# Performance work log

Hardware: AMD Instinct MI355X
Metric: run time of the kernel (lower is better)

The kernel has to match this reference:

```python
import jax, jax.numpy as jnp
import numpy as np
from jax import lax

D = 1024
N_EXP = 8
DD = 4 * D
BS = 8192
TRAIN_CAP = 1.0
LN_EPS = 1e-5


def setup_inputs() -> dict:
    key = jax.random.key(0)
    ks = jax.random.split(key, 8)
    s = 0.02
    return {
        "x": jax.random.normal(ks[0], (BS, D), jnp.float32),
        "Wg": jax.random.normal(ks[1], (N_EXP, D), jnp.float32) * s,
        "cp_w1": jax.random.normal(ks[2], (D, D), jnp.float32) * s,
        "cp_b1": jnp.zeros((D,), jnp.float32),
        "cp_w2": jax.random.normal(ks[3], (N_EXP, D), jnp.float32) * s,
        "cp_b2": jnp.zeros((N_EXP,), jnp.float32),
        "ln_g": jnp.ones((D,), jnp.float32),
        "ln_b": jnp.zeros((D,), jnp.float32),
        "fc1s": jax.random.normal(ks[4], (N_EXP, DD, D), jnp.float32) * s,
        "b1s": jnp.zeros((N_EXP, DD), jnp.float32),
        "fc2s": jax.random.normal(ks[5], (N_EXP, D, DD), jnp.float32) * s,
        "b2s": jnp.zeros((N_EXP, D), jnp.float32),
    }


def reference(x, Wg, cp_w1, cp_b1, cp_w2, cp_b2, ln_g, ln_b, fc1s, b1s, fc2s, b2s):
    bs, d = x.shape
    n = Wg.shape[0]
    k = int(bs * TRAIN_CAP) // n  # tokens kept per expert

    # gate scores in (0,1): (tanh(x Wg^T)+1)/2   -> [bs, n]
    scores = (jnp.tanh(x @ Wg.T) + 1.0) * 0.5

    # per-expert descending sort of tokens by score
    order = jnp.argsort(-scores, axis=0)                      # [bs, n]
    sorted_w = jnp.take_along_axis(scores, order, axis=0)     # [bs, n]
    kept_w = sorted_w[:k]                                     # [k, n]
    kept_idx = order[:k]                                      # [k, n]

    # keep mask (labels for capacity predictor)
    keep_mask = jnp.zeros((bs, n), x.dtype).at[kept_idx, jnp.arange(n)[None, :]].set(1.0)

    # capacity predictor loss (BCE with logits, x detached)
    xd = lax.stop_gradient(x)
    h = jax.nn.gelu(xd @ cp_w1.T + cp_b1, approximate=True)
    logits = h @ cp_w2.T + cp_b2                              # [bs, n]
    cap_loss = jnp.mean(jnp.logaddexp(0.0, logits) - logits * keep_mask)

    # dispatch: gather selected tokens, row-major flatten of [k, n]
    idx = kept_idx.reshape(-1)                                # [k*n]
    y = x[idx]                                                # [k*n, d]

    # LayerNorm
    mu = y.mean(-1, keepdims=True)
    var = y.var(-1, keepdims=True)
    y = (y - mu) * lax.rsqrt(var + LN_EPS) * ln_g + ln_b

    # per-expert grouped GEMMs
    y3 = y.reshape(k, n, d)
    h1 = jnp.einsum('knd,nfd->knf', y3, fc1s) + b1s[None]     # [k, n, dd]
    h1 = jax.nn.gelu(h1, approximate=True)
    y2 = jnp.einsum('knf,ndf->knd', h1, fc2s) + b2s[None]     # [k, n, d]

    # weight by gate score and scatter-add back (residual)
    y2 = y2 * kept_w[..., None]
    out = x.at[idx].add(y2.reshape(k * n, d))
    return out, cap_loss
```

## Files before the change

kernel.cpp:

```cpp
#include <hip/hip_runtime.h>


#define BS_   8192
#define D_    1024
#define DD_   4096
#define NEXP  8
#define KCAP  1024

typedef unsigned int   uint32;
typedef unsigned short u16;
typedef __bf16 bf16x8  __attribute__((ext_vector_type(8)));
typedef float  f32x4   __attribute__((ext_vector_type(4)));
typedef u16    u16x8   __attribute__((ext_vector_type(8)));
typedef u16    u16x4   __attribute__((ext_vector_type(4)));

__device__ __forceinline__ u16 f2bf(float f){
  uint32 u = __float_as_uint(f);
  u = (u + 0x7fffu + ((u >> 16) & 1u)) >> 16;
  return (u16)u;
}
__device__ __forceinline__ float bf_lo(uint32 u){ return __uint_as_float(u << 16); }
__device__ __forceinline__ float bf_hi(uint32 u){ return __uint_as_float(u & 0xffff0000u); }

__device__ __forceinline__ float gelu_fast(float v){
  const float u2 = v * (1.5957691216057308f + 0.07135481282962162f * v * v);
  const float e  = __expf(u2);
  return v - v / (1.0f + e);
}
__device__ __forceinline__ void glds16(const u16* g, u16* l){
  __builtin_amdgcn_global_load_lds(
      (const __attribute__((address_space(1))) unsigned int*)g,
      (__attribute__((address_space(3))) unsigned int*)l, 16, 0, 0);
}

__global__ __launch_bounds__(256)
void pack_b_kernel(const float* __restrict__ in, u16* __restrict__ out,
                   int K, int kshift)
{
  const long long t = (long long)blockIdx.x * 256 + threadIdx.x;
  const int  lane  = (int)(t & 63);
  const long long brick = t >> 6;
  const long long n16 = brick >> kshift;
  const int  k32  = (int)(brick & ((1 << kshift) - 1));
  const float* src = in + (n16 * 16 + (lane & 15)) * (long long)K
                        + k32 * 32 + (lane >> 4) * 8;
  const float4 a = *(const float4*)src;
  const float4 b = *(const float4*)(src + 4);
  u16x8 o;
  o[0]=f2bf(a.x); o[1]=f2bf(a.y); o[2]=f2bf(a.z); o[3]=f2bf(a.w);
  o[4]=f2bf(b.x); o[5]=f2bf(b.y); o[6]=f2bf(b.z); o[7]=f2bf(b.w);
  *(u16x8*)(out + t * 8) = o;
}

__global__ __launch_bounds__(64)
void gating_kernel(const float* __restrict__ x, const float* __restrict__ Wg,
                   float* __restrict__ scores, uint32* __restrict__ keep_bits,
                   u16* __restrict__ xh)
{
  const int i    = blockIdx.x;
  const int lane = threadIdx.x;
  const float* xr = x + (size_t)i * D_ + lane * 16;
  const float4 x0 = *(const float4*)(xr +  0);
  const float4 x1 = *(const float4*)(xr +  4);
  const float4 x2 = *(const float4*)(xr +  8);
  const float4 x3 = *(const float4*)(xr + 12);
  u16x8 p0, p1;
  p0[0]=f2bf(x0.x); p0[1]=f2bf(x0.y); p0[2]=f2bf(x0.z); p0[3]=f2bf(x0.w);
  p0[4]=f2bf(x1.x); p0[5]=f2bf(x1.y); p0[6]=f2bf(x1.z); p0[7]=f2bf(x1.w);
  p1[0]=f2bf(x2.x); p1[1]=f2bf(x2.y); p1[2]=f2bf(x2.z); p1[3]=f2bf(x2.w);
  p1[4]=f2bf(x3.x); p1[5]=f2bf(x3.y); p1[6]=f2bf(x3.z); p1[7]=f2bf(x3.w);
  u16* dst = xh + ((size_t)(i >> 4) * 32 + (lane >> 1)) * 512
                + (lane & 1) * 256 + (i & 15) * 8;
  *(u16x8*)dst         = p0;
  *(u16x8*)(dst + 128) = p1;

  float acc[NEXP];
  #pragma unroll
  for (int e = 0; e < NEXP; e++){
    const float* wr = Wg + e * D_ + lane * 16;
    const float4 w0 = *(const float4*)(wr +  0);
    const float4 w1 = *(const float4*)(wr +  4);
    const float4 w2 = *(const float4*)(wr +  8);
    const float4 w3 = *(const float4*)(wr + 12);
    float s = x0.x*w0.x + x0.y*w0.y + x0.z*w0.z + x0.w*w0.w;
    s += x1.x*w1.x + x1.y*w1.y + x1.z*w1.z + x1.w*w1.w;
    s += x2.x*w2.x + x2.y*w2.y + x2.z*w2.z + x2.w*w2.w;
    s += x3.x*w3.x + x3.y*w3.y + x3.z*w3.z + x3.w*w3.w;
    acc[e] = s;
  }
  #pragma unroll
  for (int e = 0; e < NEXP; e++){
    #pragma unroll
    for (int off = 32; off >= 1; off >>= 1) acc[e] += __shfl_xor(acc[e], off);
  }
  if (lane == 0){
    #pragma unroll
    for (int e = 0; e < NEXP; e++) scores[i * NEXP + e] = (tanhf(acc[e]) + 1.0f) * 0.5f;
    keep_bits[i] = 0u;
  }
}

__global__ __launch_bounds__(256)
void select_kernel(const float* __restrict__ scores, uint32* __restrict__ keep_bits,
                   int* __restrict__ counts, int* __restrict__ rowlist,
                   float* __restrict__ wlist, int* __restrict__ inv)
{
  __shared__ unsigned long long sk[2048];
  const int e = blockIdx.y;
  const int i = blockIdx.x * 256 + threadIdx.x;
  const float ms = scores[i * NEXP + e];
  const unsigned long long mk =
      ((unsigned long long)__float_as_uint(ms) << 32) | (uint32)(BS_ - 1 - i);
  int cnt = 0;
  for (int base = 0; base < BS_; base += 2048){
    #pragma unroll
    for (int u = 0; u < 8; u++){
      const int j = base + (int)threadIdx.x * 8 + u;
      const float sj = scores[j * NEXP + e];
      sk[threadIdx.x * 8 + u] =
          ((unsigned long long)__float_as_uint(sj) << 32) | (uint32)(BS_ - 1 - j);
    }
    __syncthreads();
    #pragma unroll 8
    for (int jj = 0; jj < 2048; jj++) cnt += (sk[jj] > mk) ? 1 : 0;
    __syncthreads();
  }
  if (cnt < KCAP){
    const int slot = atomicAdd(&counts[e], 1);
    rowlist[e * KCAP + slot] = i;
    wlist[e * KCAP + slot]   = ms;
    inv[i * NEXP + e]        = slot;
    atomicOr(&keep_bits[i], 1u << e);
  }
}

template<int MODE, int SPLIT>
__global__ __launch_bounds__(256)
void gemm_br(const u16* __restrict__ A, const u16* __restrict__ B,
             const float* __restrict__ bias, void* __restrict__ Cv,
             float* __restrict__ P0, float* __restrict__ P1,
             int M, int N, int K,
             long long sA, long long sB, long long sBias, long long sC)
{
  __shared__ u16 smA[8 * 512];
  __shared__ u16 smB[8 * 512];
  const int zr   = blockIdx.z;
  const int z    = zr / SPLIT, ks = zr % SPLIT;
  const int nk   = K >> 5;
  const int kIt0 = (nk / SPLIT) * ks, kIt1 = kIt0 + nk / SPLIT;
  const int m0   = blockIdx.y * 128;
  const int n0   = blockIdx.x * 128;
  const int tid  = threadIdx.x;
  const int lane = tid & 63, wv = tid >> 6;
  const int l15  = lane & 15, quad = lane >> 4;
  const int moff = (wv >> 1) * 64, noff = (wv & 1) * 64;

  const u16* Apk = A + (long long)z * sA + (long long)((m0 >> 4) + wv * 2) * nk * 512 + lane * 8;
  const u16* Bpk = B + (long long)z * sB + (long long)((n0 >> 4) + wv * 2) * nk * 512 + lane * 8;
  const long long nstr = (long long)nk * 512;

  f32x4 acc[4][4];
  #pragma unroll
  for (int i = 0; i < 4; i++)
    #pragma unroll
    for (int j = 0; j < 4; j++)
      acc[i][j] = (f32x4){0.f, 0.f, 0.f, 0.f};

  for (int kk = kIt0; kk < kIt1; kk++){
    glds16(Apk +         (long long)kk * 512, smA + (wv * 2    ) * 512);
    glds16(Apk + nstr +  (long long)kk * 512, smA + (wv * 2 + 1) * 512);
    glds16(Bpk +         (long long)kk * 512, smB + (wv * 2    ) * 512);
    glds16(Bpk + nstr +  (long long)kk * 512, smB + (wv * 2 + 1) * 512);
    __syncthreads();
    bf16x8 aF[4], bF[4];
    #pragma unroll
    for (int i = 0; i < 4; i++)
      aF[i] = *(const bf16x8*)(smA + ((wv >> 1) * 4 + i) * 512 + lane * 8);
    #pragma unroll
    for (int j = 0; j < 4; j++)
      bF[j] = *(const bf16x8*)(smB + ((wv & 1) * 4 + j) * 512 + lane * 8);
    #pragma unroll
    for (int i = 0; i < 4; i++)
      #pragma unroll
      for (int j = 0; j < 4; j++)
        acc[i][j] = __builtin_amdgcn_mfma_f32_16x16x32_bf16(bF[j], aF[i], acc[i][j], 0, 0, 0);
    __syncthreads();
  }

  if constexpr (MODE == 2){
    float* Pout = (ks == 0 ? P0 : P1) + (long long)z * sC;
    #pragma unroll
    for (int i = 0; i < 4; i++){
      const int gm = m0 + moff + i * 16 + l15;
      #pragma unroll
      for (int j = 0; j < 4; j++){
        const int gn = n0 + noff + j * 16 + quad * 4;
        *(float4*)(Pout + (long long)gm * N + gn) =
            make_float4(acc[i][j][0], acc[i][j][1], acc[i][j][2], acc[i][j][3]);
      }
    }
  } else {
    const float* biasp = bias + (long long)z * sBias;
    const long long cbase = (long long)z * sC;
    const int nkO = N >> 5;
    #pragma unroll
    for (int i = 0; i < 4; i++){
      const int gm = m0 + moff + i * 16 + l15;
      #pragma unroll
      for (int j = 0; j < 4; j++){
        const int gn = n0 + noff + j * 16 + quad * 4;
        const float4 bv = *(const float4*)(biasp + gn);
        float v0 = gelu_fast(acc[i][j][0] + bv.x);
        float v1 = gelu_fast(acc[i][j][1] + bv.y);
        float v2 = gelu_fast(acc[i][j][2] + bv.z);
        float v3 = gelu_fast(acc[i][j][3] + bv.w);
        u16x4 o; o[0]=f2bf(v0); o[1]=f2bf(v1); o[2]=f2bf(v2); o[3]=f2bf(v3);
        if constexpr (MODE == 0){
          *(u16x4*)((u16*)Cv + cbase + (long long)gm * N + gn) = o;
        } else {
          u16* dst = (u16*)Cv + cbase
                   + ((long long)(gm >> 4) * nkO + (gn >> 5)) * 512
                   + ((gn >> 3) & 3) * 128 + (gm & 15) * 8 + (gn & 7);
          *(u16x4*)dst = o;
        }
      }
    }
  }
}

__global__ __launch_bounds__(256)
void loss_kernel(const u16* __restrict__ h, const float* __restrict__ cp_w2,
                 const float* __restrict__ cp_b2, const uint32* __restrict__ keep_bits,
                 float* __restrict__ loss)
{
  __shared__ float bl;
  if (threadIdx.x == 0) bl = 0.f;
  __syncthreads();
  const int wv = threadIdx.x >> 6, lane = threadIdx.x & 63;
  const int i  = blockIdx.x * 4 + wv;
  const u16* hr = h + (size_t)i * D_ + lane * 16;
  const uint4 ha = *(const uint4*)(hr);
  const uint4 hb = *(const uint4*)(hr + 8);
  float hx[16];
  hx[0]=bf_lo(ha.x); hx[1]=bf_hi(ha.x); hx[2]=bf_lo(ha.y); hx[3]=bf_hi(ha.y);
  hx[4]=bf_lo(ha.z); hx[5]=bf_hi(ha.z); hx[6]=bf_lo(ha.w); hx[7]=bf_hi(ha.w);
  hx[8]=bf_lo(hb.x); hx[9]=bf_hi(hb.x); hx[10]=bf_lo(hb.y); hx[11]=bf_hi(hb.y);
  hx[12]=bf_lo(hb.z); hx[13]=bf_hi(hb.z); hx[14]=bf_lo(hb.w); hx[15]=bf_hi(hb.w);
  float acc[NEXP];
  #pragma unroll
  for (int e = 0; e < NEXP; e++){
    const float* wr = cp_w2 + e * D_ + lane * 16;
    const float4 w0 = *(const float4*)(wr +  0);
    const float4 w1 = *(const float4*)(wr +  4);
    const float4 w2 = *(const float4*)(wr +  8);
    const float4 w3 = *(const float4*)(wr + 12);
    float s = hx[0]*w0.x + hx[1]*w0.y + hx[2]*w0.z + hx[3]*w0.w;
    s += hx[4]*w1.x + hx[5]*w1.y + hx[6]*w1.z + hx[7]*w1.w;
    s += hx[8]*w2.x + hx[9]*w2.y + hx[10]*w2.z + hx[11]*w2.w;
    s += hx[12]*w3.x + hx[13]*w3.y + hx[14]*w3.z + hx[15]*w3.w;
    acc[e] = s;
  }
  #pragma unroll
  for (int e = 0; e < NEXP; e++){
    #pragma unroll
    for (int off = 32; off >= 1; off >>= 1) acc[e] += __shfl_xor(acc[e], off);
  }
  if (lane == 0){
    const uint32 kb = keep_bits[i];
    float li = 0.f;
    #pragma unroll
    for (int e = 0; e < NEXP; e++){
      const float l  = acc[e] + cp_b2[e];
      const float sp = fmaxf(l, 0.f) + log1pf(expf(-fabsf(l)));
      li += sp - l * (float)((kb >> e) & 1u);
    }
    atomicAdd(&bl, li);
  }
  __syncthreads();
  if (threadIdx.x == 0) atomicAdd(loss, bl);
}

__global__ __launch_bounds__(256)
void ln_gather_kernel(const float* __restrict__ x, const int* __restrict__ rowlist,
                      const float* __restrict__ ln_g, const float* __restrict__ ln_b,
                      u16* __restrict__ Y)
{
  __shared__ float red[8];
  const int b    = blockIdx.x;
  const int e    = b >> 10;
  const int slot = b & (KCAP - 1);
  const int row  = rowlist[b];
  const int tid  = threadIdx.x;
  const float4 v = *(const float4*)(x + (size_t)row * D_ + tid * 4);
  float s = v.x + v.y + v.z + v.w;
  float q = v.x*v.x + v.y*v.y + v.z*v.z + v.w*v.w;
  const int lane = tid & 63, wv = tid >> 6;
  #pragma unroll
  for (int off = 32; off >= 1; off >>= 1){ s += __shfl_xor(s, off); q += __shfl_xor(q, off); }
  if (lane == 0){ red[wv] = s; red[4 + wv] = q; }
  __syncthreads();
  s = red[0] + red[1] + red[2] + red[3];
  q = red[4] + red[5] + red[6] + red[7];
  const float mu  = s * (1.0f / D_);
  const float var = q * (1.0f / D_) - mu * mu;
  const float rs  = rsqrtf(var + 1e-5f);
  const float4 g  = *(const float4*)(ln_g + tid * 4);
  const float4 bb = *(const float4*)(ln_b + tid * 4);
  u16x4 o;
  o[0] = f2bf((v.x - mu) * rs * g.x + bb.x);
  o[1] = f2bf((v.y - mu) * rs * g.y + bb.y);
  o[2] = f2bf((v.z - mu) * rs * g.z + bb.z);
  o[3] = f2bf((v.w - mu) * rs * g.w + bb.w);
  u16* dst = Y + (size_t)e * KCAP * D_
           + ((size_t)(slot >> 4) * 32 + (tid >> 3)) * 512
           + ((tid >> 1) & 3) * 128 + (slot & 15) * 8 + (tid & 1) * 4;
  *(u16x4*)dst = o;
}

__global__ __launch_bounds__(256)
void combine_kernel(const float* __restrict__ x, const uint32* __restrict__ keep_bits,
                    const int* __restrict__ inv, const float* __restrict__ wlist,
                    const float* __restrict__ P0, const float* __restrict__ P1,
                    const float* __restrict__ b2s, float* __restrict__ out)
{
  const int i = blockIdx.x;
  const int c = threadIdx.x * 4;
  float4 v = *(const float4*)(x + (size_t)i * D_ + c);
  uint32 kb = keep_bits[i];
  while (kb){
    const int e = __ffs(kb) - 1;
    kb &= kb - 1;
    const int r = inv[i * NEXP + e];
    const float w = wlist[e * KCAP + r];
    const size_t ro = ((size_t)(e * KCAP + r)) * D_ + c;
    const float4 p0 = *(const float4*)(P0 + ro);
    const float4 p1 = *(const float4*)(P1 + ro);
    const float4 b2 = *(const float4*)(b2s + (size_t)e * D_ + c);
    v.x += w * (p0.x + p1.x + b2.x);
    v.y += w * (p0.y + p1.y + b2.y);
    v.z += w * (p0.z + p1.z + b2.z);
    v.w += w * (p0.w + p1.w + b2.w);
  }
  *(float4*)(out + (size_t)i * D_ + c) = v;
}

__global__ void finalize_loss_kernel(const float* __restrict__ loss, float* __restrict__ outp){
  outp[0] = loss[0] * (1.0f / (float)(BS_ * NEXP));
}

extern "C" void kernel_launch(void* const* d_in, const int* in_sizes, int n_in,
                              void* d_out, int out_size, void* d_ws, size_t ws_size,
                              hipStream_t stream)
{
  const float* x     = (const float*)d_in[0];
  const float* Wg    = (const float*)d_in[1];
  const float* cp_w1 = (const float*)d_in[2];
  const float* cp_b1 = (const float*)d_in[3];
  const float* cp_w2 = (const float*)d_in[4];
  const float* cp_b2 = (const float*)d_in[5];
  const float* ln_g  = (const float*)d_in[6];
  const float* ln_b  = (const float*)d_in[7];
  const float* fc1s  = (const float*)d_in[8];
  const float* b1s   = (const float*)d_in[9];
  const float* fc2s  = (const float*)d_in[10];
  const float* b2s   = (const float*)d_in[11];
  float* out = (float*)d_out;

  char* p = (char*)d_ws;
  auto take = [&](size_t bytes) -> char* {
    char* r = p; p += (bytes + 255) & ~(size_t)255; return r;
  };
  float*  scores    = (float*) take((size_t)BS_ * NEXP * 4);
  int*    counts    = (int*)   take(256);
  float*  loss      = (float*) take(256);
  int*    rowlist   = (int*)   take((size_t)BS_ * 4);
  float*  wlist     = (float*) take((size_t)BS_ * 4);
  uint32* keep_bits = (uint32*)take((size_t)BS_ * 4);
  int*    inv       = (int*)   take((size_t)BS_ * NEXP * 4);
  u16*    xh        = (u16*)   take((size_t)BS_ * D_ * 2);
  u16*    cpw1p     = (u16*)   take((size_t)D_ * D_ * 2);
  u16*    fc1p      = (u16*)   take((size_t)NEXP * DD_ * D_ * 2);
  u16*    fc2p      = (u16*)   take((size_t)NEXP * D_ * DD_ * 2);
  u16*    H1        = (u16*)   take((size_t)NEXP * KCAP * DD_ * 2);
  u16*    h_cp      = (u16*)   take((size_t)BS_ * D_ * 2);
  u16*    Y         = (u16*)   take((size_t)NEXP * KCAP * D_ * 2);
  float*  Pt0       = (float*)xh;
  float*  Pt1       = (float*)((char*)xh + ((size_t)32 << 20));

  hipMemsetAsync(counts, 0, 512, stream);

  pack_b_kernel<<<(D_ * D_ / 8) / 256, 256, 0, stream>>>(cp_w1, cpw1p, D_, 5);
  pack_b_kernel<<<(NEXP * DD_ * D_ / 8) / 256, 256, 0, stream>>>(fc1s, fc1p, D_, 5);
  pack_b_kernel<<<(NEXP * D_ * DD_ / 8) / 256, 256, 0, stream>>>(fc2s, fc2p, DD_, 7);

  gating_kernel<<<BS_, 64, 0, stream>>>(x, Wg, scores, keep_bits, xh);

  select_kernel<<<dim3(BS_ / 256, NEXP), 256, 0, stream>>>(
      scores, keep_bits, counts, rowlist, wlist, inv);

  gemm_br<0, 1><<<dim3(D_ / 128, BS_ / 128, 1), 256, 0, stream>>>(
      xh, cpw1p, cp_b1, h_cp, nullptr, nullptr, BS_, D_, D_, 0, 0, 0, 0);

  loss_kernel<<<BS_ / 4, 256, 0, stream>>>(h_cp, cp_w2, cp_b2, keep_bits, loss);

  ln_gather_kernel<<<BS_, 256, 0, stream>>>(x, rowlist, ln_g, ln_b, Y);

  gemm_br<1, 1><<<dim3(DD_ / 128, KCAP / 128, NEXP), 256, 0, stream>>>(
      Y, fc1p, b1s, H1, nullptr, nullptr, KCAP, DD_, D_,
      (long long)KCAP * D_, (long long)DD_ * D_, DD_, (long long)KCAP * DD_);

  gemm_br<2, 2><<<dim3(D_ / 128, KCAP / 128, NEXP * 2), 256, 0, stream>>>(
      H1, fc2p, nullptr, nullptr, Pt0, Pt1, KCAP, D_, DD_,
      (long long)KCAP * DD_, (long long)D_ * DD_, 0, (long long)KCAP * D_);

  combine_kernel<<<BS_, 256, 0, stream>>>(x, keep_bits, inv, wlist, Pt0, Pt1, b2s, out);

  finalize_loss_kernel<<<1, 1, 0, stream>>>(loss, out + (size_t)BS_ * D_);
}
```

Measured before the change: 917.9 us.

## Replace pairwise top-k selection with histogram threshold select; deepen GEMM k-step

New measurement: 849.7 us. 1.08x faster.

```diff
diff --git a/kernel.cpp b/kernel.cpp
--- a/kernel.cpp
+++ b/kernel.cpp
@@ -54,7 +54,7 @@
 
 __global__ __launch_bounds__(64)
 void gating_kernel(const float* __restrict__ x, const float* __restrict__ Wg,
-                   float* __restrict__ scores, uint32* __restrict__ keep_bits,
+                   float* __restrict__ scoresT, uint32* __restrict__ keep_bits,
                    u16* __restrict__ xh)
 {
   const int i    = blockIdx.x;
@@ -95,37 +95,111 @@
   }
   if (lane == 0){
     #pragma unroll
-    for (int e = 0; e < NEXP; e++) scores[i * NEXP + e] = (tanhf(acc[e]) + 1.0f) * 0.5f;
+    for (int e = 0; e < NEXP; e++) scoresT[e * BS_ + i] = (tanhf(acc[e]) + 1.0f) * 0.5f;
     keep_bits[i] = 0u;
   }
 }
 
 __global__ __launch_bounds__(256)
-void select_kernel(const float* __restrict__ scores, uint32* __restrict__ keep_bits,
-                   int* __restrict__ counts, int* __restrict__ rowlist,
-                   float* __restrict__ wlist, int* __restrict__ inv)
-{
-  __shared__ unsigned long long sk[2048];
+void sel_hist(const float* __restrict__ scoresT, uint32* __restrict__ ghist)
+{
   const int e = blockIdx.y;
   const int i = blockIdx.x * 256 + threadIdx.x;
-  const float ms = scores[i * NEXP + e];
-  const unsigned long long mk =
-      ((unsigned long long)__float_as_uint(ms) << 32) | (uint32)(BS_ - 1 - i);
-  int cnt = 0;
-  for (int base = 0; base < BS_; base += 2048){
-    #pragma unroll
-    for (int u = 0; u < 8; u++){
-      const int j = base + (int)threadIdx.x * 8 + u;
-      const float sj = scores[j * NEXP + e];
-      sk[threadIdx.x * 8 + u] =
-          ((unsigned long long)__float_as_uint(sj) << 32) | (uint32)(BS_ - 1 - j);
-    }
-    __syncthreads();
-    #pragma unroll 8
-    for (int jj = 0; jj < 2048; jj++) cnt += (sk[jj] > mk) ? 1 : 0;
-    __syncthreads();
-  }
-  if (cnt < KCAP){
+  const uint32 bits = __float_as_uint(scoresT[e * BS_ + i]);
+  atomicAdd(&ghist[((uint32)e << 19) | (bits >> 13)], 1u);
+}
+
+__global__ __launch_bounds__(256)
+void sel_thresh(const uint32* __restrict__ ghist, int* __restrict__ meta)
+{
+  __shared__ uint32 cs[256];
+  __shared__ int sh[2];
+  const int e = blockIdx.x;
+  const uint32* h = ghist + ((uint32)e << 19);
+  uint32 s = 0;
+  const int base = threadIdx.x * 2048;
+  for (int j = 0; j < 2048; j += 4){
+    const uint4 v = *(const uint4*)(h + base + j);
+    s += v.x + v.y + v.z + v.w;
+  }
+  cs[threadIdx.x] = s;
+  __syncthreads();
+  if (threadIdx.x == 0){
+    uint32 above = 0; int tc = 0;
+    for (int t = 255; t >= 0; t--){
+      if (above + cs[t] >= KCAP){ tc = t; break; }
+      above += cs[t];
+    }
+    sh[0] = tc; sh[1] = (int)above;
+  }
+  __syncthreads();
+  const int tc = sh[0];
+  const uint32 above = (uint32)sh[1];
+  uint32 s2 = 0;
+  const int b2 = tc * 2048 + threadIdx.x * 8;
+  #pragma unroll
+  for (int j = 0; j < 8; j++) s2 += h[b2 + j];
+  __syncthreads();
+  cs[threadIdx.x] = s2;
+  __syncthreads();
+  if (threadIdx.x == 0){
+    uint32 ab = above; int sc = 0;
+    for (int t = 255; t >= 0; t--){
+      if (ab + cs[t] >= KCAP){ sc = t; break; }
+      ab += cs[t];
+    }
+    int T = tc * 2048 + sc * 8;
+    for (int b = tc * 2048 + sc * 8 + 7; b >= 0; b--){
+      const uint32 hb = h[b];
+      if (ab + hb >= KCAP){ T = b; break; }
+      ab += hb;
+    }
+    meta[e * 2]     = T;
+    meta[e * 2 + 1] = KCAP - (int)ab;
+  }
+}
+
+__global__ __launch_bounds__(256)
+void sel_members(const float* __restrict__ scoresT, const int* __restrict__ meta,
+                 int* __restrict__ memcnt, int* __restrict__ memlist)
+{
+  const int e = blockIdx.y;
+  const int i = blockIdx.x * 256 + threadIdx.x;
+  const uint32 bits = __float_as_uint(scoresT[e * BS_ + i]);
+  if ((int)(bits >> 13) == meta[e * 2]){
+    const int s = atomicAdd(&memcnt[e], 1);
+    memlist[e * BS_ + s] = i;
+  }
+}
+
+__global__ __launch_bounds__(256)
+void sel_classify(const float* __restrict__ scoresT, const int* __restrict__ meta,
+                  const int* __restrict__ memcnt, const int* __restrict__ memlist,
+                  uint32* __restrict__ keep_bits, int* __restrict__ counts,
+                  int* __restrict__ rowlist, float* __restrict__ wlist,
+                  int* __restrict__ inv)
+{
+  const int e = blockIdx.y;
+  const int i = blockIdx.x * 256 + threadIdx.x;
+  const float ms = scoresT[e * BS_ + i];
+  const uint32 bits = __float_as_uint(ms);
+  const int b = (int)(bits >> 13);
+  const int T = meta[e * 2], need = meta[e * 2 + 1];
+  bool sel = (b > T);
+  if (b == T){
+    const int mc = memcnt[e];
+    if (mc <= need) sel = true;
+    else {
+      int cnt = 0;
+      for (int s = 0; s < mc; s++){
+        const int j = memlist[e * BS_ + s];
+        const uint32 bj = __float_as_uint(scoresT[e * BS_ + j]);
+        if (bj > bits || (bj == bits && j < i)) cnt++;
+      }
+      sel = (cnt < need);
+    }
+  }
+  if (sel){
     const int slot = atomicAdd(&counts[e], 1);
     rowlist[e * KCAP + slot] = i;
     wlist[e * KCAP + slot]   = ms;
@@ -135,19 +209,20 @@
 }
 
 template<int MODE, int SPLIT>
-__global__ __launch_bounds__(256)
+__global__ __launch_bounds__(256, 3)
 void gemm_br(const u16* __restrict__ A, const u16* __restrict__ B,
              const float* __restrict__ bias, void* __restrict__ Cv,
              float* __restrict__ P0, float* __restrict__ P1,
              int M, int N, int K,
              long long sA, long long sB, long long sBias, long long sC)
 {
-  __shared__ u16 smA[8 * 512];
-  __shared__ u16 smB[8 * 512];
+  __shared__ u16 smA[16 * 512];
+  __shared__ u16 smB[16 * 512];
   const int zr   = blockIdx.z;
   const int z    = zr / SPLIT, ks = zr % SPLIT;
   const int nk   = K >> 5;
-  const int kIt0 = (nk / SPLIT) * ks, kIt1 = kIt0 + nk / SPLIT;
+  const int nkk  = (K >> 6) / SPLIT;
+  const int it0  = nkk * ks;
   const int m0   = blockIdx.y * 128;
   const int n0   = blockIdx.x * 128;
   const int tid  = threadIdx.x;
@@ -155,8 +230,8 @@
   const int l15  = lane & 15, quad = lane >> 4;
   const int moff = (wv >> 1) * 64, noff = (wv & 1) * 64;
 
-  const u16* Apk = A + (long long)z * sA + (long long)((m0 >> 4) + wv * 2) * nk * 512 + lane * 8;
-  const u16* Bpk = B + (long long)z * sB + (long long)((n0 >> 4) + wv * 2) * nk * 512 + lane * 8;
+  const u16* Apk = A + (long long)z * sA + ((long long)(m0 >> 4) + wv * 2) * nk * 512 + lane * 8;
+  const u16* Bpk = B + (long long)z * sB + ((long long)(n0 >> 4) + wv * 2) * nk * 512 + lane * 8;
   const long long nstr = (long long)nk * 512;
 
   f32x4 acc[4][4];
@@ -166,24 +241,32 @@
     for (int j = 0; j < 4; j++)
       acc[i][j] = (f32x4){0.f, 0.f, 0.f, 0.f};
 
-  for (int kk = kIt0; kk < kIt1; kk++){
-    glds16(Apk +         (long long)kk * 512, smA + (wv * 2    ) * 512);
-    glds16(Apk + nstr +  (long long)kk * 512, smA + (wv * 2 + 1) * 512);
-    glds16(Bpk +         (long long)kk * 512, smB + (wv * 2    ) * 512);
-    glds16(Bpk + nstr +  (long long)kk * 512, smB + (wv * 2 + 1) * 512);
+  for (int kk = it0; kk < it0 + nkk; kk++){
+    const long long kb = (long long)(kk * 2) * 512;
+    glds16(Apk + kb,              smA + (wv * 4 + 0) * 512);
+    glds16(Apk + kb + 512,        smA + (wv * 4 + 1) * 512);
+    glds16(Apk + nstr + kb,       smA + (wv * 4 + 2) * 512);
+    glds16(Apk + nstr + kb + 512, smA + (wv * 4 + 3) * 512);
+    glds16(Bpk + kb,              smB + (wv * 4 + 0) * 512);
+    glds16(Bpk + kb + 512,        smB + (wv * 4 + 1) * 512);
+    glds16(Bpk + nstr + kb,       smB + (wv * 4 + 2) * 512);
+    glds16(Bpk + nstr + kb + 512, smB + (wv * 4 + 3) * 512);
     __syncthreads();
-    bf16x8 aF[4], bF[4];
-    #pragma unroll
-    for (int i = 0; i < 4; i++)
-      aF[i] = *(const bf16x8*)(smA + ((wv >> 1) * 4 + i) * 512 + lane * 8);
-    #pragma unroll
-    for (int j = 0; j < 4; j++)
-      bF[j] = *(const bf16x8*)(smB + ((wv & 1) * 4 + j) * 512 + lane * 8);
-    #pragma unroll
-    for (int i = 0; i < 4; i++)
+    #pragma unroll
+    for (int kh = 0; kh < 2; kh++){
+      bf16x8 aF[4], bF[4];
+      #pragma unroll
+      for (int i = 0; i < 4; i++)
+        aF[i] = *(const bf16x8*)(smA + ((((wv >> 1) * 4 + i) * 2 + kh) * 512) + lane * 8);
       #pragma unroll
       for (int j = 0; j < 4; j++)
-        acc[i][j] = __builtin_amdgcn_mfma_f32_16x16x32_bf16(bF[j], aF[i], acc[i][j], 0, 0, 0);
+        bF[j] = *(const bf16x8*)(smB + ((((wv & 1) * 4 + j) * 2 + kh) * 512) + lane * 8);
+      #pragma unroll
+      for (int i = 0; i < 4; i++)
+        #pragma unroll
+        for (int j = 0; j < 4; j++)
+          acc[i][j] = __builtin_amdgcn_mfma_f32_16x16x32_bf16(bF[j], aF[i], acc[i][j], 0, 0, 0);
+    }
     __syncthreads();
   }
 
@@ -370,9 +453,10 @@
   auto take = [&](size_t bytes) -> char* {
     char* r = p; p += (bytes + 255) & ~(size_t)255; return r;
   };
-  float*  scores    = (float*) take((size_t)BS_ * NEXP * 4);
+  float*  scoresT   = (float*) take((size_t)BS_ * NEXP * 4);
   int*    counts    = (int*)   take(256);
   float*  loss      = (float*) take(256);
+  int*    meta      = (int*)   take(256);
   int*    rowlist   = (int*)   take((size_t)BS_ * 4);
   float*  wlist     = (float*) take((size_t)BS_ * 4);
   uint32* keep_bits = (uint32*)take((size_t)BS_ * 4);
@@ -384,19 +468,26 @@
   u16*    H1        = (u16*)   take((size_t)NEXP * KCAP * DD_ * 2);
   u16*    h_cp      = (u16*)   take((size_t)BS_ * D_ * 2);
   u16*    Y         = (u16*)   take((size_t)NEXP * KCAP * D_ * 2);
+  int*    memcnt    = meta + 16;
+  uint32* ghist     = (uint32*)H1;
+  int*    memlist   = (int*)((char*)H1 + ((size_t)16 << 20));
   float*  Pt0       = (float*)xh;
   float*  Pt1       = (float*)((char*)xh + ((size_t)32 << 20));
 
-  hipMemsetAsync(counts, 0, 512, stream);
+  hipMemsetAsync(counts, 0, 768, stream);
+  hipMemsetAsync(ghist, 0, (size_t)16 << 20, stream);
 
   pack_b_kernel<<<(D_ * D_ / 8) / 256, 256, 0, stream>>>(cp_w1, cpw1p, D_, 5);
   pack_b_kernel<<<(NEXP * DD_ * D_ / 8) / 256, 256, 0, stream>>>(fc1s, fc1p, D_, 5);
   pack_b_kernel<<<(NEXP * D_ * DD_ / 8) / 256, 256, 0, stream>>>(fc2s, fc2p, DD_, 7);
 
-  gating_kernel<<<BS_, 64, 0, stream>>>(x, Wg, scores, keep_bits, xh);
-
-  select_kernel<<<dim3(BS_ / 256, NEXP), 256, 0, stream>>>(
-      scores, keep_bits, counts, rowlist, wlist, inv);
+  gating_kernel<<<BS_, 64, 0, stream>>>(x, Wg, scoresT, keep_bits, xh);
+
+  sel_hist    <<<dim3(BS_ / 256, NEXP), 256, 0, stream>>>(scoresT, ghist);
+  sel_thresh  <<<NEXP, 256, 0, stream>>>(ghist, meta);
+  sel_members <<<dim3(BS_ / 256, NEXP), 256, 0, stream>>>(scoresT, meta, memcnt, memlist);
+  sel_classify<<<dim3(BS_ / 256, NEXP), 256, 0, stream>>>(
+      scoresT, meta, memcnt, memlist, keep_bits, counts, rowlist, wlist, inv);
 
   gemm_br<0, 1><<<dim3(D_ / 128, BS_ / 128, 1), 256, 0, stream>>>(
       xh, cpw1p, cp_b1, h_cp, nullptr, nullptr, BS_, D_, D_, 0, 0, 0, 0);
```
